# Performance work log

Hardware: AMD Instinct MI355X
Metric: run time of the kernel (lower is better)

## Reference

```python
import jax, jax.numpy as jnp
import numpy as np

EPS = 1e-5

# ---------------- numpy-side hash/index precomputation ----------------

def _key(c):
    c = c.astype(np.int64) + 2  # shift so all coords >= 0
    return (c[..., 0] * 4096 + c[..., 1]) * 4096 + c[..., 2]

def _lookup(table_keys, query_keys):
    order = np.argsort(table_keys)
    sk = table_keys[order]
    pos = np.clip(np.searchsorted(sk, query_keys), 0, len(sk) - 1)
    found = sk[pos] == query_keys
    return np.where(found, order[pos], -1).astype(np.int64)

def setup_inputs() -> dict:
    N, C_IN, C_OUT, RES = 400_000, 32, 64, 1.0
    rng = np.random.default_rng(0)
    coords = rng.uniform(0.0, 100.0, (N, 3)).astype(np.float32)
    pf = rng.standard_normal((N, C_IN)).astype(np.float32)

    # initial_voxelize: unique voxel coords + point->voxel map
    vc = np.floor(coords / RES).astype(np.int64)
    uv, p2v_in = np.unique(vc, axis=0, return_inverse=True)
    p2v_in = p2v_in.reshape(-1)
    cnt_in = np.bincount(p2v_in, minlength=len(uv)).astype(np.float32)

    # strided conv output lattice (stride 2)
    ouv = np.unique(uv // 2, axis=0)
    ikeys, okeys = _key(uv), _key(ouv)

    # kernel-2 stride-2 conv map: input voxel at 2*out + off, off in {0,1}^3
    offs2 = np.array([[i, j, k] for i in (0, 1) for j in (0, 1) for k in (0, 1)], np.int64)
    conv_map = np.stack([_lookup(ikeys, _key(ouv * 2 + o)) for o in offs2], axis=1)

    # kernel-3 neighbor map on the output lattice
    offs3 = np.array([[i, j, k] for i in (-1, 0, 1) for j in (-1, 0, 1) for k in (-1, 0, 1)], np.int64)
    nbr27 = np.stack([_lookup(okeys, _key(ouv + o)) for o in offs3], axis=1)

    # trilinear voxel_to_point on output lattice (voxel size = 2*RES)
    q = coords / (2.0 * RES)
    base = np.floor(q).astype(np.int64)
    frac = (q - base).astype(np.float32)
    tri_idx, tri_w = [], []
    for o in offs2:
        idx = _lookup(okeys, _key(base + o))
        w = np.prod(np.where(o[None, :] == 1, frac, 1.0 - frac), axis=1).astype(np.float32)
        tri_idx.append(idx)
        tri_w.append(np.where(idx >= 0, w, 0.0).astype(np.float32))
    tri_idx = np.stack(tri_idx, axis=1)
    tri_w = np.stack(tri_w, axis=1)

    # point_to_voxel: containing output voxel (always exists)
    p2v_out = _lookup(okeys, _key(base))
    cnt_out = np.bincount(p2v_out, minlength=len(ouv)).astype(np.float32)

    def glorot(r, *shape):
        fan_in = shape[-2] * int(np.prod(shape[:-2])) if len(shape) > 2 else shape[0]
        return (r.standard_normal(shape) / np.sqrt(fan_in)).astype(np.float32)

    return dict(
        pf=jnp.asarray(pf),
        Wc=jnp.asarray(glorot(rng, 8, C_IN, C_OUT)),
        g1=jnp.ones(C_OUT, jnp.float32), b1=jnp.zeros(C_OUT, jnp.float32),
        Wr1=jnp.asarray(glorot(rng, 27, C_OUT, C_OUT)),
        gr1=jnp.ones(C_OUT, jnp.float32), br1=jnp.zeros(C_OUT, jnp.float32),
        Wr2=jnp.asarray(glorot(rng, 27, C_OUT, C_OUT)),
        gr2=jnp.ones(C_OUT, jnp.float32), br2=jnp.zeros(C_OUT, jnp.float32),
        Wpt=jnp.asarray(glorot(rng, C_OUT, C_OUT)), bpt=jnp.zeros(C_OUT, jnp.float32),
        gp=jnp.ones(C_OUT, jnp.float32), bp=jnp.zeros(C_OUT, jnp.float32),
        tri_w=jnp.asarray(tri_w), cnt_in=jnp.asarray(cnt_in), cnt_out=jnp.asarray(cnt_out),
        p2v_in=jnp.asarray(p2v_in), conv_map=jnp.asarray(conv_map),
        nbr27=jnp.asarray(nbr27), tri_idx=jnp.asarray(tri_idx), p2v_out=jnp.asarray(p2v_out),
    )

# ---------------- jax forward ----------------

def _bn(x, g, b):  # training-mode batch norm over voxel/point dim
    m = x.mean(0)
    v = x.var(0)
    return (x - m) * jax.lax.rsqrt(v + EPS) * g + b

def _seg_mean(x, seg, cnt):  # spvoxelize: scatter-mean
    return jax.ops.segment_sum(x, seg, num_segments=cnt.shape[0]) / cnt[:, None]

def _sconv(f, nbr, W):  # sparse conv: per-offset gather + matmul accumulate
    out = jnp.zeros((nbr.shape[0], W.shape[2]), f.dtype)
    for k in range(W.shape[0]):
        idx = nbr[:, k]
        g = jnp.where((idx >= 0)[:, None], f[jnp.maximum(idx, 0)], 0.0)
        out = out + g @ W[k]
    return out

def _tri(f, idx, w):  # trilinear voxel->point gather (w already 0 for missing)
    out = jnp.zeros((idx.shape[0], f.shape[1]), f.dtype)
    for j in range(idx.shape[1]):
        out = out + w[:, j:j + 1] * f[jnp.maximum(idx[:, j], 0)]
    return out

def reference(pf, Wc, g1, b1, Wr1, gr1, br1, Wr2, gr2, br2, Wpt, bpt, gp, bp,
              tri_w, cnt_in, cnt_out, p2v_in, conv_map, nbr27, tri_idx, p2v_out):
    vf0 = _seg_mean(pf, p2v_in, cnt_in)                         # initial_voxelize [M_in,32]
    vf1 = jax.nn.relu(_bn(_sconv(vf0, conv_map, Wc), g1, b1))   # conv_in [M_out,64]
    pfeat = _tri(vf1, tri_idx, tri_w)                           # voxel_to_point [N,64]
    vf2 = _seg_mean(pfeat, p2v_out, cnt_out)                    # point_to_voxel [M_out,64]
    h = jax.nn.relu(_bn(_sconv(vf2, nbr27, Wr1), gr1, br1))     # ResBlock conv1
    h = jax.nn.relu(_bn(_sconv(h, nbr27, Wr2), gr2, br2))       # ResBlock conv2
    vf3 = h + vf2                                               # residual sum
    p_out = jax.nn.relu(_bn(pfeat @ Wpt + bpt, gp, bp))         # point_layer
    pfeat2 = _tri(vf3, tri_idx, tri_w) + p_out                  # v2p + fuse
    vf4 = _seg_mean(pfeat2, p2v_out, cnt_out)                   # point_to_voxel
    return vf4, pfeat2
```

## Files before the change

### kernel.cpp

```cpp
#include <hip/hip_runtime.h>

#define EPSV 1e-5f
#define CDIV(a, b) (((a) + (b) - 1) / (b))

using short8 = __attribute__((ext_vector_type(8))) short;
using f32x4 = __attribute__((ext_vector_type(4))) float;

__device__ __forceinline__ unsigned short bf16rne(float x) {
  unsigned u = __float_as_uint(x);
  unsigned r = (u + 0x7fffu + ((u >> 16) & 1u)) >> 16;
  return (unsigned short)r;
}

__global__ void k_scatter_in(const float* __restrict__ pf, const int* __restrict__ p2v,
                             float* __restrict__ vf0, int total) {
  int i = blockIdx.x * 256 + threadIdx.x;
  if (i >= total) return;
  atomicAdd(&vf0[(size_t)p2v[i >> 5] * 32 + (i & 31)], pf[i]);
}

__global__ void k_div_in(float* __restrict__ vf0, const float* __restrict__ cnt, int total) {
  int i = blockIdx.x * 256 + threadIdx.x;
  if (i >= total) return;
  vf0[i] /= cnt[i >> 5];
}

__global__ __launch_bounds__(256) void k_conv1(const float* __restrict__ vin,
                                               const int* __restrict__ cmap,
                                               const float* __restrict__ W,
                                               float* __restrict__ out,
                                               float* __restrict__ stats, int Vout) {
  __shared__ float fs[32][128];
  __shared__ float Ws[32 * 64];
  __shared__ int idxs[128 * 8];
  __shared__ float ss[128];
  const int tid = threadIdx.x;
  const int vb = blockIdx.x * 128;
  for (int i = tid; i < 128 * 8; i += 256) {
    int g = vb * 8 + i;
    idxs[i] = (g < Vout * 8) ? cmap[g] : -1;
  }
  if (tid < 128) ss[tid] = 0.f;
  const int vq = tid & 15, cq = tid >> 4;
  const int v0 = vq * 8, c0 = cq * 4;
  const int srow = tid & 127, sci = (tid >> 7) * 16;
  float acc[8][4];
#pragma unroll
  for (int r = 0; r < 8; ++r)
#pragma unroll
    for (int q = 0; q < 4; ++q) acc[r][q] = 0.f;

  for (int k = 0; k < 8; ++k) {
    __syncthreads();
    for (int i = tid; i < 32 * 64; i += 256) Ws[i] = W[k * 2048 + i];
    int idx = idxs[srow * 8 + k];
    if (idx >= 0) {
#pragma unroll
      for (int j = 0; j < 16; j += 4) {
        float4 t = *(const float4*)&vin[(size_t)idx * 32 + sci + j];
        fs[sci + j + 0][srow] = t.x;
        fs[sci + j + 1][srow] = t.y;
        fs[sci + j + 2][srow] = t.z;
        fs[sci + j + 3][srow] = t.w;
      }
    } else {
#pragma unroll
      for (int j = 0; j < 16; ++j) fs[sci + j][srow] = 0.f;
    }
    __syncthreads();
#pragma unroll 8
    for (int ci = 0; ci < 32; ++ci) {
      float4 w4 = *(const float4*)&Ws[ci * 64 + c0];
      float4 fa = *(const float4*)&fs[ci][v0];
      float4 fb = *(const float4*)&fs[ci][v0 + 4];
      float fv[8] = {fa.x, fa.y, fa.z, fa.w, fb.x, fb.y, fb.z, fb.w};
      float wv[4] = {w4.x, w4.y, w4.z, w4.w};
#pragma unroll
      for (int r = 0; r < 8; ++r)
#pragma unroll
        for (int q = 0; q < 4; ++q) acc[r][q] += fv[r] * wv[q];
    }
  }
  float s1[4] = {0, 0, 0, 0}, s2[4] = {0, 0, 0, 0};
#pragma unroll
  for (int r = 0; r < 8; ++r) {
    int v = vb + v0 + r;
    if (v < Vout) {
      *(float4*)&out[(size_t)v * 64 + c0] =
          make_float4(acc[r][0], acc[r][1], acc[r][2], acc[r][3]);
#pragma unroll
      for (int q = 0; q < 4; ++q) {
        float x = acc[r][q];
        s1[q] += x;
        s2[q] += x * x;
      }
    }
  }
#pragma unroll
  for (int q = 0; q < 4; ++q) {
    atomicAdd(&ss[c0 + q], s1[q]);
    atomicAdd(&ss[64 + c0 + q], s2[q]);
  }
  __syncthreads();
  if (tid < 128) atomicAdd(&stats[tid], ss[tid]);
}

__global__ void k_bnfin(const float* __restrict__ stats, const float* __restrict__ g,
                        const float* __restrict__ b, float* __restrict__ sb, int rows) {
  int c = threadIdx.x;
  float inv = 1.f / (float)rows;
  float m = stats[c] * inv;
  float v = stats[64 + c] * inv - m * m;
  float sc = g[c] * rsqrtf(v + EPSV);
  sb[c] = sc;
  sb[64 + c] = b[c] - m * sc;
}

__global__ __launch_bounds__(1024) void k_scan_part(const float* __restrict__ cnt,
                                                    int* __restrict__ partial, int V) {
  __shared__ int s[1024];
  int i = blockIdx.x * 1024 + threadIdx.x;
  s[threadIdx.x] = (i < V) ? (int)cnt[i] : 0;
  __syncthreads();
  for (int st = 512; st > 0; st >>= 1) {
    if (threadIdx.x < st) s[threadIdx.x] += s[threadIdx.x + st];
    __syncthreads();
  }
  if (threadIdx.x == 0) partial[blockIdx.x] = s[0];
}

__global__ __launch_bounds__(1024) void k_scan_top(int* __restrict__ partial, int nb) {
  __shared__ int s[1024];
  int t = threadIdx.x;
  int orig = (t < nb) ? partial[t] : 0;
  s[t] = orig;
  __syncthreads();
  for (int st = 1; st < 1024; st <<= 1) {
    int v = (t >= st) ? s[t - st] : 0;
    __syncthreads();
    s[t] += v;
    __syncthreads();
  }
  if (t < nb) partial[t] = s[t] - orig;
}

__global__ __launch_bounds__(1024) void k_scan_write(const float* __restrict__ cnt,
                                                     const int* __restrict__ partial,
                                                     int* __restrict__ starts,
                                                     int* __restrict__ cursor, int V) {
  __shared__ int s[1024];
  int t = threadIdx.x;
  int i = blockIdx.x * 1024 + t;
  int orig = (i < V) ? (int)cnt[i] : 0;
  s[t] = orig;
  __syncthreads();
  for (int st = 1; st < 1024; st <<= 1) {
    int v = (t >= st) ? s[t - st] : 0;
    __syncthreads();
    s[t] += v;
    __syncthreads();
  }
  if (i < V) {
    int excl = s[t] - orig + partial[blockIdx.x];
    starts[i] = excl;
    cursor[i] = excl;
  }
}

__global__ void k_bucket(const int* __restrict__ p2v, int* __restrict__ cursor,
                         int* __restrict__ plist, int N) {
  int p = blockIdx.x * 256 + threadIdx.x;
  if (p >= N) return;
  int pos = atomicAdd(&cursor[p2v[p]], 1);
  plist[pos] = p;
}

__global__ __launch_bounds__(256) void k_tri1v(const float* __restrict__ c1,
                                               const float* __restrict__ sb0,
                                               const int* __restrict__ tidx,
                                               const float* __restrict__ twt,
                                               const int* __restrict__ starts,
                                               const float* __restrict__ cnt,
                                               const int* __restrict__ plist,
                                               float* __restrict__ pfeat,
                                               float* __restrict__ vf2, int V) {
  int t = threadIdx.x;
  int v = blockIdx.x * 4 + (t >> 6);
  int c = t & 63;
  if (v >= V) return;
  int s0 = starts[v];
  int n = (int)cnt[v];
  if (n < 1) return;
  int p0 = plist[s0];
  float sc = sb0[c], bi = sb0[64 + c];
  float R[8];
#pragma unroll
  for (int j = 0; j < 8; ++j) {
    int idx = tidx[(size_t)p0 * 8 + j];
    R[j] = (idx >= 0) ? fmaxf(sc * c1[(size_t)idx * 64 + c] + bi, 0.f) : 0.f;
  }
  float acc_v = 0.f;
  for (int i = 0; i < n; ++i) {
    int p = plist[s0 + i];
    float4 w0 = *(const float4*)&twt[(size_t)p * 8];
    float4 w1 = *(const float4*)&twt[(size_t)p * 8 + 4];
    float acc = w0.x * R[0] + w0.y * R[1] + w0.z * R[2] + w0.w * R[3] +
                w1.x * R[4] + w1.y * R[5] + w1.z * R[6] + w1.w * R[7];
    pfeat[(size_t)p * 64 + c] = acc;
    acc_v += acc;
  }
  vf2[(size_t)v * 64 + c] = acc_v / (float)n;
}

__global__ void k_wprep(const float* __restrict__ W, short* __restrict__ Wh,
                        short* __restrict__ Wl, int ntap) {
  int t = blockIdx.x * 256 + threadIdx.x;
  int total = ntap * 2 * 4 * 64;
  if (t >= total) return;
  int l = t & 63;
  int n = (t >> 6) & 3;
  int s = (t >> 8) & 1;
  int k = t >> 9;
  int co = n * 16 + (l & 15);
  int ci0 = s * 32 + (l >> 4) * 8;
#pragma unroll
  for (int j = 0; j < 8; ++j) {
    float x = W[((size_t)(k * 64 + ci0 + j)) * 64 + co];
    unsigned short hb = bf16rne(x);
    float hf = __uint_as_float((unsigned)hb << 16);
    Wh[(size_t)t * 8 + j] = (short)hb;
    Wl[(size_t)t * 8 + j] = (short)bf16rne(x - hf);
  }
}

__global__ void k_split(const float* __restrict__ in, const float* __restrict__ sb,
                        short* __restrict__ packed, int total) {
  int i = blockIdx.x * 256 + threadIdx.x;
  if (i >= total) return;
  int c = i & 63;
  float x = in[i];
  if (sb) x = fmaxf(sb[c] * x + sb[64 + c], 0.f);
  unsigned short hb = bf16rne(x);
  float hf = __uint_as_float((unsigned)hb << 16);
  size_t base = (size_t)(i >> 6) * 128 + c;
  packed[base] = (short)hb;
  packed[base + 64] = (short)bf16rne(x - hf);
}

__global__ __launch_bounds__(256) void k_conv27r(const short* __restrict__ A_g,
                                                 const int* __restrict__ nbr,
                                                 const short* __restrict__ Wh,
                                                 const short* __restrict__ Wl,
                                                 float* __restrict__ out,
                                                 float* __restrict__ stats, int Vout) {
  __shared__ float ss[128];
  const int tid = threadIdx.x;
  const int lane = tid & 63;
  const int w = tid >> 6;
  const int vb = blockIdx.x * 128 + w * 32;
  if (tid < 128) ss[tid] = 0.f;
  const int vv = lane & 15, kq = lane >> 4;
  const int v0 = vb + vv, v1 = vb + 16 + vv;
  const bool ok0 = v0 < Vout, ok1 = v1 < Vout;
  const int koff = kq * 8;

  f32x4 acc[2][4];
#pragma unroll
  for (int m = 0; m < 2; ++m)
#pragma unroll
    for (int n = 0; n < 4; ++n)
#pragma unroll
      for (int r = 0; r < 4; ++r) acc[m][n][r] = 0.f;

  auto ldA = [&](int idx, int off) -> short8 {
    if (idx < 0) {
      short8 z = 0;
      return z;
    }
    return *(const short8*)&A_g[(size_t)idx * 128 + off];
  };

  short8 cA[8], nA[8];
  int idn0, idn1;

  {
    int i0 = ok0 ? nbr[(size_t)v0 * 27] : -1;
    int i1 = ok1 ? nbr[(size_t)v1 * 27] : -1;
#pragma unroll
    for (int s = 0; s < 2; ++s)
#pragma unroll
      for (int h = 0; h < 2; ++h) {
        cA[s * 2 + h] = ldA(i0, h * 64 + s * 32 + koff);
        cA[4 + s * 2 + h] = ldA(i1, h * 64 + s * 32 + koff);
      }
    idn0 = ok0 ? nbr[(size_t)v0 * 27 + 1] : -1;
    idn1 = ok1 ? nbr[(size_t)v1 * 27 + 1] : -1;
  }

  for (int k = 0; k < 27; ++k) {
    int idf0 = -1, idf1 = -1;
    if (k + 1 < 27) {
#pragma unroll
      for (int s = 0; s < 2; ++s)
#pragma unroll
        for (int h = 0; h < 2; ++h) {
          nA[s * 2 + h] = ldA(idn0, h * 64 + s * 32 + koff);
          nA[4 + s * 2 + h] = ldA(idn1, h * 64 + s * 32 + koff);
        }
      if (k + 2 < 27) {
        idf0 = ok0 ? nbr[(size_t)v0 * 27 + (k + 2)] : -1;
        idf1 = ok1 ? nbr[(size_t)v1 * 27 + (k + 2)] : -1;
      }
    }
    const short* bkh = Wh + (size_t)k * 4096 + lane * 8;
    const short* bkl = Wl + (size_t)k * 4096 + lane * 8;
#pragma unroll
    for (int s = 0; s < 2; ++s) {
      short8 ah0 = cA[s * 2], al0 = cA[s * 2 + 1];
      short8 ah1 = cA[4 + s * 2], al1 = cA[4 + s * 2 + 1];
#pragma unroll
      for (int n = 0; n < 4; ++n) {
        short8 bh = *(const short8*)&bkh[(s * 4 + n) * 512];
        short8 bl = *(const short8*)&bkl[(s * 4 + n) * 512];
        acc[0][n] = __builtin_amdgcn_mfma_f32_16x16x32_bf16(ah0, bh, acc[0][n], 0, 0, 0);
        acc[0][n] = __builtin_amdgcn_mfma_f32_16x16x32_bf16(al0, bh, acc[0][n], 0, 0, 0);
        acc[0][n] = __builtin_amdgcn_mfma_f32_16x16x32_bf16(ah0, bl, acc[0][n], 0, 0, 0);
        acc[1][n] = __builtin_amdgcn_mfma_f32_16x16x32_bf16(ah1, bh, acc[1][n], 0, 0, 0);
        acc[1][n] = __builtin_amdgcn_mfma_f32_16x16x32_bf16(al1, bh, acc[1][n], 0, 0, 0);
        acc[1][n] = __builtin_amdgcn_mfma_f32_16x16x32_bf16(ah1, bl, acc[1][n], 0, 0, 0);
      }
    }
    if (k + 1 < 27) {
#pragma unroll
      for (int q = 0; q < 8; ++q) cA[q] = nA[q];
      idn0 = idf0;
      idn1 = idf1;
    }
  }

  const int col = lane & 15, rq = lane >> 4;
  __syncthreads();
#pragma unroll
  for (int m = 0; m < 2; ++m) {
#pragma unroll
    for (int n = 0; n < 4; ++n) {
      int c = n * 16 + col;
      float s1 = 0.f, s2 = 0.f;
#pragma unroll
      for (int r = 0; r < 4; ++r) {
        int v = vb + m * 16 + rq * 4 + r;
        if (v < Vout) {
          float x = acc[m][n][r];
          out[(size_t)v * 64 + c] = x;
          s1 += x;
          s2 += x * x;
        }
      }
      atomicAdd(&ss[c], s1);
      atomicAdd(&ss[64 + c], s2);
    }
  }
  __syncthreads();
  if (tid < 128) atomicAdd(&stats[tid], ss[tid]);
}

__global__ void k_vf3(const float* __restrict__ h2, const float* __restrict__ vf2,
                      const float* __restrict__ sb2, float* __restrict__ vf3, int total) {
  int i = blockIdx.x * 256 + threadIdx.x;
  if (i >= total) return;
  int c = i & 63;
  vf3[i] = fmaxf(sb2[c] * h2[i] + sb2[64 + c], 0.f) + vf2[i];
}

__global__ __launch_bounds__(256) void k_pmm(const float* __restrict__ pfeat,
                                             const float* __restrict__ Wpt,
                                             const float* __restrict__ bpt,
                                             float* __restrict__ outbuf,
                                             float* __restrict__ stats, int N) {
  __shared__ float fs[64][128];
  __shared__ float Ws[64 * 64];
  __shared__ float ss[128];
  const int tid = threadIdx.x;
  const int pb = blockIdx.x * 128;
  for (int i = tid; i < 64 * 64; i += 256) Ws[i] = Wpt[i];
  if (tid < 128) ss[tid] = 0.f;
  const int srow = tid & 127, sci = (tid >> 7) * 32;
  int p = pb + srow;
  if (p < N) {
#pragma unroll
    for (int j = 0; j < 32; j += 4) {
      float4 t = *(const float4*)&pfeat[(size_t)p * 64 + sci + j];
      fs[sci + j + 0][srow] = t.x;
      fs[sci + j + 1][srow] = t.y;
      fs[sci + j + 2][srow] = t.z;
      fs[sci + j + 3][srow] = t.w;
    }
  } else {
#pragma unroll
    for (int j = 0; j < 32; ++j) fs[sci + j][srow] = 0.f;
  }
  __syncthreads();
  const int vq = tid & 15, cq = tid >> 4;
  const int p0 = vq * 8, c0 = cq * 4;
  float acc[8][4];
#pragma unroll
  for (int r = 0; r < 8; ++r)
#pragma unroll
    for (int q = 0; q < 4; ++q) acc[r][q] = 0.f;
#pragma unroll 8
  for (int ci = 0; ci < 64; ++ci) {
    float4 w4 = *(const float4*)&Ws[ci * 64 + c0];
    float4 fa = *(const float4*)&fs[ci][p0];
    float4 fb = *(const float4*)&fs[ci][p0 + 4];
    float fv[8] = {fa.x, fa.y, fa.z, fa.w, fb.x, fb.y, fb.z, fb.w};
    float wv[4] = {w4.x, w4.y, w4.z, w4.w};
#pragma unroll
    for (int r = 0; r < 8; ++r)
#pragma unroll
      for (int q = 0; q < 4; ++q) acc[r][q] += fv[r] * wv[q];
  }
  float bb[4] = {bpt[c0], bpt[c0 + 1], bpt[c0 + 2], bpt[c0 + 3]};
  float s1[4] = {0, 0, 0, 0}, s2[4] = {0, 0, 0, 0};
#pragma unroll
  for (int r = 0; r < 8; ++r) {
    int pp = pb + p0 + r;
    if (pp < N) {
      float4 o;
      o.x = acc[r][0] + bb[0];
      o.y = acc[r][1] + bb[1];
      o.z = acc[r][2] + bb[2];
      o.w = acc[r][3] + bb[3];
      *(float4*)&outbuf[(size_t)pp * 64 + c0] = o;
      s1[0] += o.x; s2[0] += o.x * o.x;
      s1[1] += o.y; s2[1] += o.y * o.y;
      s1[2] += o.z; s2[2] += o.z * o.z;
      s1[3] += o.w; s2[3] += o.w * o.w;
    }
  }
#pragma unroll
  for (int q = 0; q < 4; ++q) {
    atomicAdd(&ss[c0 + q], s1[q]);
    atomicAdd(&ss[64 + c0 + q], s2[q]);
  }
  __syncthreads();
  if (tid < 128) atomicAdd(&stats[tid], ss[tid]);
}

__global__ __launch_bounds__(256) void k_tri2v(const float* __restrict__ vf3,
                                               const float* __restrict__ sb3,
                                               const int* __restrict__ tidx,
                                               const float* __restrict__ twt,
                                               const int* __restrict__ starts,
                                               const float* __restrict__ cnt,
                                               const int* __restrict__ plist,
                                               float* __restrict__ pf2,
                                               float* __restrict__ vf4, int V) {
  int t = threadIdx.x;
  int v = blockIdx.x * 4 + (t >> 6);
  int c = t & 63;
  if (v >= V) return;
  int s0 = starts[v];
  int n = (int)cnt[v];
  if (n < 1) return;
  int p0 = plist[s0];
  float S[8];
#pragma unroll
  for (int j = 0; j < 8; ++j) {
    int idx = tidx[(size_t)p0 * 8 + j];
    S[j] = (idx >= 0) ? vf3[(size_t)idx * 64 + c] : 0.f;
  }
  float s3 = sb3[c], b3 = sb3[64 + c];
  float acc_v = 0.f;
  for (int i = 0; i < n; ++i) {
    int p = plist[s0 + i];
    float4 w0 = *(const float4*)&twt[(size_t)p * 8];
    float4 w1 = *(const float4*)&twt[(size_t)p * 8 + 4];
    float raw = pf2[(size_t)p * 64 + c];
    float val = fmaxf(s3 * raw + b3, 0.f) +
                w0.x * S[0] + w0.y * S[1] + w0.z * S[2] + w0.w * S[3] +
                w1.x * S[4] + w1.y * S[5] + w1.z * S[6] + w1.w * S[7];
    pf2[(size_t)p * 64 + c] = val;
    acc_v += val;
  }
  vf4[(size_t)v * 64 + c] = acc_v / (float)n;
}

extern "C" void kernel_launch(void* const* d_in, const int* in_sizes, int n_in,
                              void* d_out, int out_size, void* d_ws, size_t ws_size,
                              hipStream_t stream) {
  const float* pf = (const float*)d_in[0];
  const float* Wc = (const float*)d_in[1];
  const float* g1 = (const float*)d_in[2];
  const float* b1 = (const float*)d_in[3];
  const float* Wr1 = (const float*)d_in[4];
  const float* gr1 = (const float*)d_in[5];
  const float* br1 = (const float*)d_in[6];
  const float* Wr2 = (const float*)d_in[7];
  const float* gr2 = (const float*)d_in[8];
  const float* br2 = (const float*)d_in[9];
  const float* Wpt = (const float*)d_in[10];
  const float* bpt = (const float*)d_in[11];
  const float* gp = (const float*)d_in[12];
  const float* bp = (const float*)d_in[13];
  const float* twt = (const float*)d_in[14];
  const float* cnt_in = (const float*)d_in[15];
  const float* cnt_out = (const float*)d_in[16];
  const int* p2v_in = (const int*)d_in[17];
  const int* conv_map = (const int*)d_in[18];
  const int* nbr27 = (const int*)d_in[19];
  const int* tri_idx = (const int*)d_in[20];
  const int* p2v_out = (const int*)d_in[21];

  const int N = in_sizes[0] / 32;
  const int Vin = in_sizes[15];
  const int Vout = in_sizes[16];

  float* ws = (float*)d_ws;
  size_t o = 0;
  auto alloc = [&](size_t nf) {
    float* pbase = ws + o;
    o += (nf + 63) & ~(size_t)63;
    return pbase;
  };
  size_t vf0_sz = (size_t)Vin * 32;
  size_t vf3_sz = (size_t)Vout * 64;
  float* vf0 = alloc(vf0_sz > vf3_sz ? vf0_sz : vf3_sz);
  float* c1 = alloc((size_t)Vout * 64);
  float* pfeat = alloc((size_t)N * 64);
  float* vf2 = alloc((size_t)Vout * 64);
  float* h1 = alloc((size_t)Vout * 64);
  float* stats = alloc(512);
  float* sb = alloc(512);
  int* partial = (int*)alloc(1024);
  int* starts = (int*)alloc(Vout);
  int* cursor = (int*)alloc(Vout);
  int* plist = (int*)alloc(N);
  const int WFRAG = 27 * 2 * 4 * 64 * 8;
  short* Wh1 = (short*)alloc(WFRAG / 2);
  short* Wl1 = (short*)alloc(WFRAG / 2);
  short* Wh2 = (short*)alloc(WFRAG / 2);
  short* Wl2 = (short*)alloc(WFRAG / 2);
  float* vf3 = vf0;
  float* h2 = c1;
  short* vf2p = (short*)pfeat;
  short* h1p = vf2p + (size_t)Vout * 128;

  float* vf4 = (float*)d_out;
  float* pf2 = vf4 + (size_t)Vout * 64;

  const int nb = CDIV(Vout, 1024);

  hipMemsetAsync(vf0, 0, (size_t)Vin * 32 * sizeof(float), stream);
  hipMemsetAsync(stats, 0, 512 * sizeof(float), stream);

  k_scatter_in<<<CDIV(N * 32, 256), 256, 0, stream>>>(pf, p2v_in, vf0, N * 32);
  k_div_in<<<CDIV(Vin * 32, 256), 256, 0, stream>>>(vf0, cnt_in, Vin * 32);
  k_conv1<<<CDIV(Vout, 128), 256, 0, stream>>>(vf0, conv_map, Wc, c1, stats, Vout);
  k_bnfin<<<1, 64, 0, stream>>>(stats, g1, b1, sb, Vout);

  k_scan_part<<<nb, 1024, 0, stream>>>(cnt_out, partial, Vout);
  k_scan_top<<<1, 1024, 0, stream>>>(partial, nb);
  k_scan_write<<<nb, 1024, 0, stream>>>(cnt_out, partial, starts, cursor, Vout);
  k_bucket<<<CDIV(N, 256), 256, 0, stream>>>(p2v_out, cursor, plist, N);

  k_wprep<<<CDIV(27 * 2 * 4 * 64, 256), 256, 0, stream>>>(Wr1, Wh1, Wl1, 27);
  k_wprep<<<CDIV(27 * 2 * 4 * 64, 256), 256, 0, stream>>>(Wr2, Wh2, Wl2, 27);

  k_tri1v<<<CDIV(Vout, 4), 256, 0, stream>>>(c1, sb, tri_idx, twt, starts, cnt_out,
                                             plist, pfeat, vf2, Vout);

  k_pmm<<<CDIV(N, 128), 256, 0, stream>>>(pfeat, Wpt, bpt, pf2, stats + 384, N);
  k_bnfin<<<1, 64, 0, stream>>>(stats + 384, gp, bp, sb + 384, N);

  k_split<<<CDIV(Vout * 64, 256), 256, 0, stream>>>(vf2, nullptr, vf2p, Vout * 64);
  k_conv27r<<<CDIV(Vout, 128), 256, 0, stream>>>(vf2p, nbr27, Wh1, Wl1, h1,
                                                 stats + 128, Vout);
  k_bnfin<<<1, 64, 0, stream>>>(stats + 128, gr1, br1, sb + 128, Vout);

  k_split<<<CDIV(Vout * 64, 256), 256, 0, stream>>>(h1, sb + 128, h1p, Vout * 64);
  k_conv27r<<<CDIV(Vout, 128), 256, 0, stream>>>(h1p, nbr27, Wh2, Wl2, h2,
                                                 stats + 256, Vout);
  k_bnfin<<<1, 64, 0, stream>>>(stats + 256, gr2, br2, sb + 256, Vout);

  k_vf3<<<CDIV(Vout * 64, 256), 256, 0, stream>>>(h2, vf2, sb + 256, vf3, Vout * 64);

  k_tri2v<<<CDIV(Vout, 4), 256, 0, stream>>>(vf3, sb + 384, tri_idx, twt, starts,
                                             cnt_out, plist, pf2, vf4, Vout);
}
```

Baseline: 1.236 ms.

## Replace atomic input voxelization with bucketed gather; swizzle conv27 blocks across XCDs

Measured after the change: 1.311 ms. 1.06x slower.

```diff
diff --git a/kernel.cpp b/kernel.cpp
--- a/kernel.cpp
+++ b/kernel.cpp
@@ -10,19 +10,6 @@
   unsigned u = __float_as_uint(x);
   unsigned r = (u + 0x7fffu + ((u >> 16) & 1u)) >> 16;
   return (unsigned short)r;
-}
-
-__global__ void k_scatter_in(const float* __restrict__ pf, const int* __restrict__ p2v,
-                             float* __restrict__ vf0, int total) {
-  int i = blockIdx.x * 256 + threadIdx.x;
-  if (i >= total) return;
-  atomicAdd(&vf0[(size_t)p2v[i >> 5] * 32 + (i & 31)], pf[i]);
-}
-
-__global__ void k_div_in(float* __restrict__ vf0, const float* __restrict__ cnt, int total) {
-  int i = blockIdx.x * 256 + threadIdx.x;
-  if (i >= total) return;
-  vf0[i] /= cnt[i >> 5];
 }
 
 __global__ __launch_bounds__(256) void k_conv1(const float* __restrict__ vin,
@@ -173,6 +160,22 @@
   if (p >= N) return;
   int pos = atomicAdd(&cursor[p2v[p]], 1);
   plist[pos] = p;
+}
+
+__global__ __launch_bounds__(256) void k_seg_gather_in(const float* __restrict__ src,
+                                                       const int* __restrict__ starts,
+                                                       const float* __restrict__ cnt,
+                                                       const int* __restrict__ plist,
+                                                       float* __restrict__ dst, int V) {
+  int t = threadIdx.x;
+  int v = blockIdx.x * 8 + (t >> 5);
+  int c = t & 31;
+  if (v >= V) return;
+  int s0 = starts[v];
+  int n = (int)cnt[v];
+  float acc = 0.f;
+  for (int i = 0; i < n; ++i) acc += src[(size_t)plist[s0 + i] * 32 + c];
+  dst[(size_t)v * 32 + c] = acc / (float)n;
 }
 
 __global__ __launch_bounds__(256) void k_tri1v(const float* __restrict__ c1,
@@ -247,18 +250,23 @@
   packed[base + 64] = (short)bf16rne(x - hf);
 }
 
-__global__ __launch_bounds__(256) void k_conv27r(const short* __restrict__ A_g,
+__global__ __launch_bounds__(128) void k_conv27r(const short* __restrict__ A_g,
                                                  const int* __restrict__ nbr,
                                                  const short* __restrict__ Wh,
                                                  const short* __restrict__ Wl,
                                                  float* __restrict__ out,
-                                                 float* __restrict__ stats, int Vout) {
+                                                 float* __restrict__ stats, int Vout,
+                                                 int nwg) {
   __shared__ float ss[128];
   const int tid = threadIdx.x;
   const int lane = tid & 63;
   const int w = tid >> 6;
-  const int vb = blockIdx.x * 128 + w * 32;
-  if (tid < 128) ss[tid] = 0.f;
+  int bid = blockIdx.x;
+  int q = nwg >> 3, r = nwg & 7;
+  int xcd = bid & 7, pos = bid >> 3;
+  int swz = (xcd < r ? xcd * (q + 1) : r * (q + 1) + (xcd - r) * q) + pos;
+  const int vb = swz * 64 + w * 32;
+  ss[tid] = 0.f;
   const int vv = lane & 15, kq = lane >> 4;
   const int v0 = vb + vv, v1 = vb + 16 + vv;
   const bool ok0 = v0 < Vout, ok1 = v1 < Vout;
@@ -270,7 +278,7 @@
 #pragma unroll
     for (int n = 0; n < 4; ++n)
 #pragma unroll
-      for (int r = 0; r < 4; ++r) acc[m][n][r] = 0.f;
+      for (int rr = 0; rr < 4; ++rr) acc[m][n][rr] = 0.f;
 
   auto ldA = [&](int idx, int off) -> short8 {
     if (idx < 0) {
@@ -332,7 +340,7 @@
     }
     if (k + 1 < 27) {
 #pragma unroll
-      for (int q = 0; q < 8; ++q) cA[q] = nA[q];
+      for (int qq = 0; qq < 8; ++qq) cA[qq] = nA[qq];
       idn0 = idf0;
       idn1 = idf1;
     }
@@ -347,10 +355,10 @@
       int c = n * 16 + col;
       float s1 = 0.f, s2 = 0.f;
 #pragma unroll
-      for (int r = 0; r < 4; ++r) {
-        int v = vb + m * 16 + rq * 4 + r;
+      for (int rr = 0; rr < 4; ++rr) {
+        int v = vb + w * 0 + m * 16 + rq * 4 + rr;
         if (v < Vout) {
-          float x = acc[m][n][r];
+          float x = acc[m][n][rr];
           out[(size_t)v * 64 + c] = x;
           s1 += x;
           s2 += x * x;
@@ -361,7 +369,7 @@
     }
   }
   __syncthreads();
-  if (tid < 128) atomicAdd(&stats[tid], ss[tid]);
+  atomicAdd(&stats[tid], ss[tid]);
 }
 
 __global__ void k_vf3(const float* __restrict__ h2, const float* __restrict__ vf2,
@@ -535,6 +543,9 @@
   int* starts = (int*)alloc(Vout);
   int* cursor = (int*)alloc(Vout);
   int* plist = (int*)alloc(N);
+  int* starts_in = (int*)alloc(Vin);
+  int* cursor_in = (int*)alloc(Vin);
+  int* plist_in = (int*)alloc(N);
   const int WFRAG = 27 * 2 * 4 * 64 * 8;
   short* Wh1 = (short*)alloc(WFRAG / 2);
   short* Wl1 = (short*)alloc(WFRAG / 2);
@@ -548,19 +559,25 @@
   float* vf4 = (float*)d_out;
   float* pf2 = vf4 + (size_t)Vout * 64;
 
-  const int nb = CDIV(Vout, 1024);
-
-  hipMemsetAsync(vf0, 0, (size_t)Vin * 32 * sizeof(float), stream);
+  const int nb_out = CDIV(Vout, 1024);
+  const int nb_in = CDIV(Vin, 1024);
+  const int nwg27 = CDIV(Vout, 64);
+
   hipMemsetAsync(stats, 0, 512 * sizeof(float), stream);
 
-  k_scatter_in<<<CDIV(N * 32, 256), 256, 0, stream>>>(pf, p2v_in, vf0, N * 32);
-  k_div_in<<<CDIV(Vin * 32, 256), 256, 0, stream>>>(vf0, cnt_in, Vin * 32);
+  k_scan_part<<<nb_in, 1024, 0, stream>>>(cnt_in, partial, Vin);
+  k_scan_top<<<1, 1024, 0, stream>>>(partial, nb_in);
+  k_scan_write<<<nb_in, 1024, 0, stream>>>(cnt_in, partial, starts_in, cursor_in, Vin);
+  k_bucket<<<CDIV(N, 256), 256, 0, stream>>>(p2v_in, cursor_in, plist_in, N);
+  k_seg_gather_in<<<CDIV(Vin, 8), 256, 0, stream>>>(pf, starts_in, cnt_in, plist_in,
+                                                    vf0, Vin);
+
   k_conv1<<<CDIV(Vout, 128), 256, 0, stream>>>(vf0, conv_map, Wc, c1, stats, Vout);
   k_bnfin<<<1, 64, 0, stream>>>(stats, g1, b1, sb, Vout);
 
-  k_scan_part<<<nb, 1024, 0, stream>>>(cnt_out, partial, Vout);
-  k_scan_top<<<1, 1024, 0, stream>>>(partial, nb);
-  k_scan_write<<<nb, 1024, 0, stream>>>(cnt_out, partial, starts, cursor, Vout);
+  k_scan_part<<<nb_out, 1024, 0, stream>>>(cnt_out, partial, Vout);
+  k_scan_top<<<1, 1024, 0, stream>>>(partial, nb_out);
+  k_scan_write<<<nb_out, 1024, 0, stream>>>(cnt_out, partial, starts, cursor, Vout);
   k_bucket<<<CDIV(N, 256), 256, 0, stream>>>(p2v_out, cursor, plist, N);
 
   k_wprep<<<CDIV(27 * 2 * 4 * 64, 256), 256, 0, stream>>>(Wr1, Wh1, Wl1, 27);
@@ -573,13 +590,13 @@
   k_bnfin<<<1, 64, 0, stream>>>(stats + 384, gp, bp, sb + 384, N);
 
   k_split<<<CDIV(Vout * 64, 256), 256, 0, stream>>>(vf2, nullptr, vf2p, Vout * 64);
-  k_conv27r<<<CDIV(Vout, 128), 256, 0, stream>>>(vf2p, nbr27, Wh1, Wl1, h1,
-                                                 stats + 128, Vout);
+  k_conv27r<<<nwg27, 128, 0, stream>>>(vf2p, nbr27, Wh1, Wl1, h1, stats + 128, Vout,
+                                       nwg27);
   k_bnfin<<<1, 64, 0, stream>>>(stats + 128, gr1, br1, sb + 128, Vout);
 
   k_split<<<CDIV(Vout * 64, 256), 256, 0, stream>>>(h1, sb + 128, h1p, Vout * 64);
-  k_conv27r<<<CDIV(Vout, 128), 256, 0, stream>>>(h1p, nbr27, Wh2, Wl2, h2,
-                                                 stats + 256, Vout);
+  k_conv27r<<<nwg27, 128, 0, stream>>>(h1p, nbr27, Wh2, Wl2, h2, stats + 256, Vout,
+                                       nwg27);
   k_bnfin<<<1, 64, 0, stream>>>(stats + 256, gr2, br2, sb + 256, Vout);
 
   k_vf3<<<CDIV(Vout * 64, 256), 256, 0, stream>>>(h2, vf2, sb + 256, vf3, Vout * 64);
```
